# Kernel optimization log

Hardware: AMD Instinct MI355X
Metric: run time of the kernel (lower is better)

The kernel has to match this reference:

```python
import jax, jax.numpy as jnp
import numpy as np

B, T, F, H, NQ = 256, 512, 128, 256, 4


def setup_inputs() -> dict:
    key = jax.random.key(0)
    ks = jax.random.split(key, 7)
    s = 0.1
    return {
        "x": jax.random.normal(ks[0], (B, T, F), dtype=jnp.float32),
        "W_in": jax.random.normal(ks[1], (F + H, NQ), dtype=jnp.float32) * s,
        "b_in": jax.random.normal(ks[2], (NQ,), dtype=jnp.float32) * s,
        "Wq": jax.random.normal(ks[3], (4, NQ, NQ), dtype=jnp.float32) * s,
        "bq": jax.random.normal(ks[4], (4, NQ), dtype=jnp.float32) * s,
        "W_out": jax.random.normal(ks[5], (NQ, H), dtype=jnp.float32) * s,
        "b_out": jax.random.normal(ks[6], (H,), dtype=jnp.float32) * s,
    }


def reference(x, W_in, b_in, Wq, bq, W_out, b_out):
    # x: [B, T, F] (batch_first). Sequential LSTM-like recurrence via lax.scan.
    batch = x.shape[0]
    hidden = W_out.shape[1]

    def step(carry, x_t):
        h, c = carry
        v = jnp.concatenate([h, x_t], axis=1)              # [B, H+F]
        y = v @ W_in + b_in                                # [B, NQ]
        # 4 VQC branches (classical surrogate: tanh(linear)), vectorized over k
        q = jnp.tanh(jnp.einsum('bq,kqr->kbr', y, Wq) + bq[:, None, :])  # [4, B, NQ]
        z = jnp.einsum('kbq,qh->kbh', q, W_out) + b_out    # [4, B, H]
        i = jax.nn.sigmoid(z[0])
        f = jax.nn.sigmoid(z[1])
        g = jnp.tanh(z[2])
        o = jax.nn.sigmoid(z[3])
        c = f * c + i * g
        h = o * jnp.tanh(c)
        return (h, c), h

    h0 = jnp.zeros((batch, hidden), dtype=x.dtype)
    c0 = jnp.zeros((batch, hidden), dtype=x.dtype)
    (h_T, c_T), hs = jax.lax.scan(step, (h0, c0), jnp.swapaxes(x, 0, 1))
    hidden_seq = jnp.swapaxes(hs, 0, 1)                    # [B, T, H]
    return hidden_seq, (h_T, c_T)
```

## Files before the change

### kernel.cpp

```cpp
#include <hip/hip_runtime.h>


#define B_ 256
#define T_ 512
#define F_ 128
#define H_ 256

#define SC1 1.442695041f
#define SC2 2.885390082f
#define ISC2 0.3465735903f

typedef float f2 __attribute__((ext_vector_type(2)));

__device__ __forceinline__ float rcp_f(float x)  { return __builtin_amdgcn_rcpf(x); }
__device__ __forceinline__ float exp2_f(float x) { return __builtin_amdgcn_exp2f(x); }

__device__ __forceinline__ f2 mk2(float a, float b) { f2 v; v.x = a; v.y = b; return v; }

__device__ __forceinline__ float rl(float v, int lane) {
    return __int_as_float(__builtin_amdgcn_readlane(__float_as_int(v), lane));
}

__device__ __forceinline__ void tree4(float& p0, float& p1, float& p2, float& p3) {
    asm volatile(
        "s_nop 1\n\t"
        "v_add_f32_dpp %0, %0, %0 quad_perm:[1,0,3,2] row_mask:0xf bank_mask:0xf\n\t"
        "v_add_f32_dpp %1, %1, %1 quad_perm:[1,0,3,2] row_mask:0xf bank_mask:0xf\n\t"
        "v_add_f32_dpp %2, %2, %2 quad_perm:[1,0,3,2] row_mask:0xf bank_mask:0xf\n\t"
        "v_add_f32_dpp %3, %3, %3 quad_perm:[1,0,3,2] row_mask:0xf bank_mask:0xf\n\t"
        "v_add_f32_dpp %0, %0, %0 quad_perm:[2,3,0,1] row_mask:0xf bank_mask:0xf\n\t"
        "v_add_f32_dpp %1, %1, %1 quad_perm:[2,3,0,1] row_mask:0xf bank_mask:0xf\n\t"
        "v_add_f32_dpp %2, %2, %2 quad_perm:[2,3,0,1] row_mask:0xf bank_mask:0xf\n\t"
        "v_add_f32_dpp %3, %3, %3 quad_perm:[2,3,0,1] row_mask:0xf bank_mask:0xf\n\t"
        "v_add_f32_dpp %0, %0, %0 row_half_mirror row_mask:0xf bank_mask:0xf\n\t"
        "v_add_f32_dpp %1, %1, %1 row_half_mirror row_mask:0xf bank_mask:0xf\n\t"
        "v_add_f32_dpp %2, %2, %2 row_half_mirror row_mask:0xf bank_mask:0xf\n\t"
        "v_add_f32_dpp %3, %3, %3 row_half_mirror row_mask:0xf bank_mask:0xf\n\t"
        "v_add_f32_dpp %0, %0, %0 row_mirror row_mask:0xf bank_mask:0xf\n\t"
        "v_add_f32_dpp %1, %1, %1 row_mirror row_mask:0xf bank_mask:0xf\n\t"
        "v_add_f32_dpp %2, %2, %2 row_mirror row_mask:0xf bank_mask:0xf\n\t"
        "v_add_f32_dpp %3, %3, %3 row_mirror row_mask:0xf bank_mask:0xf\n\t"
        "v_add_f32_dpp %0, %0, %0 row_bcast:15 row_mask:0xf bank_mask:0xf\n\t"
        "v_add_f32_dpp %1, %1, %1 row_bcast:15 row_mask:0xf bank_mask:0xf\n\t"
        "v_add_f32_dpp %2, %2, %2 row_bcast:15 row_mask:0xf bank_mask:0xf\n\t"
        "v_add_f32_dpp %3, %3, %3 row_bcast:15 row_mask:0xf bank_mask:0xf\n\t"
        "v_add_f32_dpp %0, %0, %0 row_bcast:31 row_mask:0xf bank_mask:0xf\n\t"
        "v_add_f32_dpp %1, %1, %1 row_bcast:31 row_mask:0xf bank_mask:0xf\n\t"
        "v_add_f32_dpp %2, %2, %2 row_bcast:31 row_mask:0xf bank_mask:0xf\n\t"
        "v_add_f32_dpp %3, %3, %3 row_bcast:31 row_mask:0xf bank_mask:0xf"
        : "+v"(p0), "+v"(p1), "+v"(p2), "+v"(p3));
}

__device__ __forceinline__ void lds_barrier() {
    asm volatile("s_waitcnt lgkmcnt(0)\n\ts_barrier" ::: "memory");
}

__global__ __launch_bounds__(256, 1) void qlstm_kernel(
    const float* __restrict__ x,
    const float* __restrict__ W_in,
    const float* __restrict__ b_in,
    const float* __restrict__ Wq,
    const float* __restrict__ bq,
    const float* __restrict__ W_out,
    const float* __restrict__ b_out,
    float* __restrict__ out)
{
    const int b = blockIdx.x;
    const int g = threadIdx.x;
    const int w = g >> 6;
    const int l = g & 63;

    __shared__ float4 part[2][4];

    const float4* Win4 = (const float4*)W_in;

    float4 t4 = Win4[g];
    float wh[4] = {t4.x, t4.y, t4.z, t4.w};

    const bool has_x = (w < 2);
    float wx[4] = {0.f, 0.f, 0.f, 0.f};
    if (has_x) {
        float4 u4 = Win4[H_ + g];
        wx[0] = u4.x; wx[1] = u4.y; wx[2] = u4.z; wx[3] = u4.w;
    }

    const float sk[4] = {-SC1, -SC1, SC2, -SC1};
    float wo_k[4][4];
    float bo_k[4];
    {
        const float bo = b_out[g];
#pragma unroll
        for (int r = 0; r < 4; ++r) {
            const float wor = W_out[r * H_ + g];
#pragma unroll
            for (int k = 0; k < 4; ++k) wo_k[k][r] = wor * sk[k];
        }
#pragma unroll
        for (int k = 0; k < 4; ++k) bo_k[k] = bo * sk[k];
    }

    float bin[4];
#pragma unroll
    for (int q = 0; q < 4; ++q) bin[q] = b_in[q];

    const int m = l & 15, qk = m >> 2, qr = m & 3;
    float wql[4];
#pragma unroll
    for (int s = 0; s < 4; ++s) wql[s] = Wq[qk * 16 + s * 4 + qr];
    float bql = bq[qk * 4 + qr];
#pragma unroll
    for (int s = 0; s < 4; ++s) bql = fmaf(bin[s], wql[s], bql);
    bql *= SC2;
#pragma unroll
    for (int s = 0; s < 4; ++s) wql[s] *= SC2;

    float h = 0.f;
    float C = 0.f;

    const float* xp = x + (size_t)b * T_ * F_ + g;
    float xq0 = 0.f, xq1 = 0.f, xq2 = 0.f, xq3 = 0.f;
    float xv1 = 0.f;
    if (has_x) {
        const float xv0 = xp[0];
        xv1 = xp[F_];
        xq0 = xv0 * wx[0]; xq1 = xv0 * wx[1];
        xq2 = xv0 * wx[2]; xq3 = xv0 * wx[3];
    }

    float* outp = out + (size_t)b * T_ * H_ + g;

#define STEP(t, slot)                                                          \
    {                                                                          \
        float p0 = fmaf(h, wh[0], xq0);                                        \
        float p1 = fmaf(h, wh[1], xq1);                                        \
        float p2 = fmaf(h, wh[2], xq2);                                        \
        float p3 = fmaf(h, wh[3], xq3);                                        \
        tree4(p0, p1, p2, p3);                                                 \
        if (l == 63) part[slot][w] = make_float4(p0, p1, p2, p3);              \
        lds_barrier();                                                         \
        const float4 a0 = part[slot][0];                                       \
        const float4 a1 = part[slot][1];                                       \
        const float4 a2 = part[slot][2];                                       \
        const float4 a3 = part[slot][3];                                       \
         \
        if (has_x) {                                                           \
            xq0 = xv1 * wx[0]; xq1 = xv1 * wx[1];                              \
            xq2 = xv1 * wx[2]; xq3 = xv1 * wx[3];                              \
            int tn = (t) + 2; if (tn >= T_) tn = T_ - 1;                       \
            xv1 = xp[(size_t)tn * F_];                                         \
        }                                                                      \
        const f2 y01 = (mk2(a0.x, a0.y) + mk2(a1.x, a1.y)) +                   \
                       (mk2(a2.x, a2.y) + mk2(a3.x, a3.y));                    \
        const f2 y23 = (mk2(a0.z, a0.w) + mk2(a1.z, a1.w)) +                   \
                       (mk2(a2.z, a2.w) + mk2(a3.z, a3.w));                    \
        float u = fmaf(y01.x, wql[0], bql);                                    \
        const float vv = fmaf(y23.x, wql[2], y01.y * wql[1]);                  \
        u = fmaf(y23.y, wql[3], u);                                            \
        const float aq = u + vv;                                               \
        const float qown = 1.0f - 2.0f * rcp_f(1.0f + exp2_f(aq));             \
        float qs[16];                                                          \
        _Pragma("unroll")                                                      \
        for (int i = 0; i < 16; ++i) qs[i] = rl(qown, i);                      \
        float zp[4];                                                           \
        _Pragma("unroll")                                                      \
        for (int k = 0; k < 4; ++k) {                                          \
            float a = fmaf(qs[k * 4 + 0], wo_k[k][0], bo_k[k]);                \
            const float bs = fmaf(qs[k * 4 + 1], wo_k[k][1],                   \
                                  qs[k * 4 + 2] * wo_k[k][2]);                 \
            a = fmaf(qs[k * 4 + 3], wo_k[k][3], a);                            \
            zp[k] = a + bs;                                                    \
        }                                                                      \
        const float e0 = exp2_f(zp[0]);                                        \
        const float e1 = exp2_f(zp[1]);                                        \
        const float E2 = exp2_f(zp[2]);                                        \
        const float e3 = exp2_f(zp[3]);                                        \
        const float num2 = fmaf(SC2, E2, -SC2);                                \
        const float IG2  = num2 * rcp_f((1.0f + e0) * (1.0f + E2));            \
        const float fg   = rcp_f(1.0f + e1);                                   \
        C = fmaf(fg, C, IG2);                                                  \
        const float Ec = exp2_f(C);                                            \
        h = (Ec - 1.0f) * rcp_f((1.0f + e3) * (1.0f + Ec));                    \
        outp[(size_t)(t) * H_] = h;                                            \
    }

    for (int t = 0; t < T_; t += 2) {
        STEP(t, 0);
        STEP(t + 1, 1);
    }
#undef STEP

    float* hT = out + (size_t)B_ * T_ * H_;
    hT[(size_t)b * H_ + g] = h;
    hT[(size_t)B_ * H_ + (size_t)b * H_ + g] = C * ISC2;
}

extern "C" void kernel_launch(void* const* d_in, const int* in_sizes, int n_in,
                              void* d_out, int out_size, void* d_ws, size_t ws_size,
                              hipStream_t stream) {
    const float* x     = (const float*)d_in[0];
    const float* W_in  = (const float*)d_in[1];
    const float* b_in  = (const float*)d_in[2];
    const float* Wq    = (const float*)d_in[3];
    const float* bq    = (const float*)d_in[4];
    const float* W_out = (const float*)d_in[5];
    const float* b_out = (const float*)d_in[6];
    float* out = (float*)d_out;

    qlstm_kernel<<<dim3(B_), dim3(256), 0, stream>>>(
        x, W_in, b_in, Wq, bq, W_out, b_out, out);
}
```

Baseline: 369.9 us.

## Fold Wq projection before LDS exchange and shorten critical-path algebra

Result: no change. 369.9 us (+0.0%).

```diff
diff --git a/kernel.cpp b/kernel.cpp
--- a/kernel.cpp
+++ b/kernel.cpp
@@ -10,12 +10,8 @@
 #define SC2 2.885390082f
 #define ISC2 0.3465735903f
 
-typedef float f2 __attribute__((ext_vector_type(2)));
-
 __device__ __forceinline__ float rcp_f(float x)  { return __builtin_amdgcn_rcpf(x); }
 __device__ __forceinline__ float exp2_f(float x) { return __builtin_amdgcn_exp2f(x); }
-
-__device__ __forceinline__ f2 mk2(float a, float b) { f2 v; v.x = a; v.y = b; return v; }
 
 __device__ __forceinline__ float rl(float v, int lane) {
     return __int_as_float(__builtin_amdgcn_readlane(__float_as_int(v), lane));
@@ -70,7 +66,7 @@
     const int w = g >> 6;
     const int l = g & 63;
 
-    __shared__ float4 part[2][4];
+    __shared__ float partA[2][16][4];
 
     const float4* Win4 = (const float4*)W_in;
 
@@ -85,18 +81,20 @@
     }
 
     const float sk[4] = {-SC1, -SC1, SC2, -SC1};
-    float wo_k[4][4];
-    float bo_k[4];
+    float wo2[4][4];
+    float bo2[4];
     {
         const float bo = b_out[g];
-#pragma unroll
-        for (int r = 0; r < 4; ++r) {
-            const float wor = W_out[r * H_ + g];
-#pragma unroll
-            for (int k = 0; k < 4; ++k) wo_k[k][r] = wor * sk[k];
+        float wos[4];
+        float wsum = 0.f;
+#pragma unroll
+        for (int r = 0; r < 4; ++r) { wos[r] = W_out[r * H_ + g]; wsum += wos[r]; }
+#pragma unroll
+        for (int k = 0; k < 4; ++k) {
+            bo2[k] = sk[k] * (bo + wsum);
+#pragma unroll
+            for (int r = 0; r < 4; ++r) wo2[k][r] = -2.0f * sk[k] * wos[r];
         }
-#pragma unroll
-        for (int k = 0; k < 4; ++k) bo_k[k] = bo * sk[k];
     }
 
     float bin[4];
@@ -113,9 +111,10 @@
     bql *= SC2;
 #pragma unroll
     for (int s = 0; s < 4; ++s) wql[s] *= SC2;
-
-    float h = 0.f;
-    float C = 0.f;
+    const float bqlw = (w == 0) ? bql : 0.0f;
+
+    float tau = 0.f, C = 0.f;
+    float owh0 = 0.f, owh1 = 0.f, owh2 = 0.f, owh3 = 0.f;
 
     const float* xp = x + (size_t)b * T_ * F_ + g;
     float xq0 = 0.f, xq1 = 0.f, xq2 = 0.f, xq3 = 0.f;
@@ -128,20 +127,23 @@
     }
 
     float* outp = out + (size_t)b * T_ * H_ + g;
+    float o_last = 0.f;
 
 #define STEP(t, slot)                                                          \
     {                                                                          \
-        float p0 = fmaf(h, wh[0], xq0);                                        \
-        float p1 = fmaf(h, wh[1], xq1);                                        \
-        float p2 = fmaf(h, wh[2], xq2);                                        \
-        float p3 = fmaf(h, wh[3], xq3);                                        \
+        float p0 = fmaf(tau, owh0, xq0);                                       \
+        float p1 = fmaf(tau, owh1, xq1);                                       \
+        float p2 = fmaf(tau, owh2, xq2);                                       \
+        float p3 = fmaf(tau, owh3, xq3);                                       \
         tree4(p0, p1, p2, p3);                                                 \
-        if (l == 63) part[slot][w] = make_float4(p0, p1, p2, p3);              \
+                \
+        float u = fmaf(p0, wql[0], bqlw);                                      \
+        const float vv = fmaf(p3, wql[3], p2 * wql[2]);                        \
+        u = fmaf(p1, wql[1], u);                                               \
+        const float aqw = u + vv;                                              \
+        if (l >= 48) partA[slot][m][w] = aqw;                                  \
         lds_barrier();                                                         \
-        const float4 a0 = part[slot][0];                                       \
-        const float4 a1 = part[slot][1];                                       \
-        const float4 a2 = part[slot][2];                                       \
-        const float4 a3 = part[slot][3];                                       \
+        const float4 a = *(const float4*)&partA[slot][m][0];                   \
          \
         if (has_x) {                                                           \
             xq0 = xv1 * wx[0]; xq1 = xv1 * wx[1];                              \
@@ -149,26 +151,19 @@
             int tn = (t) + 2; if (tn >= T_) tn = T_ - 1;                       \
             xv1 = xp[(size_t)tn * F_];                                         \
         }                                                                      \
-        const f2 y01 = (mk2(a0.x, a0.y) + mk2(a1.x, a1.y)) +                   \
-                       (mk2(a2.x, a2.y) + mk2(a3.x, a3.y));                    \
-        const f2 y23 = (mk2(a0.z, a0.w) + mk2(a1.z, a1.w)) +                   \
-                       (mk2(a2.z, a2.w) + mk2(a3.z, a3.w));                    \
-        float u = fmaf(y01.x, wql[0], bql);                                    \
-        const float vv = fmaf(y23.x, wql[2], y01.y * wql[1]);                  \
-        u = fmaf(y23.y, wql[3], u);                                            \
-        const float aq = u + vv;                                               \
-        const float qown = 1.0f - 2.0f * rcp_f(1.0f + exp2_f(aq));             \
+        const float aq = (a.x + a.y) + (a.z + a.w);                            \
+        const float qp = rcp_f(1.0f + exp2_f(aq));     \
         float qs[16];                                                          \
         _Pragma("unroll")                                                      \
-        for (int i = 0; i < 16; ++i) qs[i] = rl(qown, i);                      \
+        for (int i = 0; i < 16; ++i) qs[i] = rl(qp, i);                        \
         float zp[4];                                                           \
         _Pragma("unroll")                                                      \
         for (int k = 0; k < 4; ++k) {                                          \
-            float a = fmaf(qs[k * 4 + 0], wo_k[k][0], bo_k[k]);                \
-            const float bs = fmaf(qs[k * 4 + 1], wo_k[k][1],                   \
-                                  qs[k * 4 + 2] * wo_k[k][2]);                 \
-            a = fmaf(qs[k * 4 + 3], wo_k[k][3], a);                            \
-            zp[k] = a + bs;                                                    \
+            float za = fmaf(qs[k * 4 + 0], wo2[k][0], bo2[k]);                 \
+            const float zb = fmaf(qs[k * 4 + 1], wo2[k][1],                    \
+                                  qs[k * 4 + 2] * wo2[k][2]);                  \
+            za = fmaf(qs[k * 4 + 3], wo2[k][3], za);                           \
+            zp[k] = za + zb;                                                   \
         }                                                                      \
         const float e0 = exp2_f(zp[0]);                                        \
         const float e1 = exp2_f(zp[1]);                                        \
@@ -178,9 +173,14 @@
         const float IG2  = num2 * rcp_f((1.0f + e0) * (1.0f + E2));            \
         const float fg   = rcp_f(1.0f + e1);                                   \
         C = fmaf(fg, C, IG2);                                                  \
+                \
+        const float o = rcp_f(1.0f + e3);                                      \
+        owh0 = o * wh[0]; owh1 = o * wh[1];                                    \
+        owh2 = o * wh[2]; owh3 = o * wh[3];                                    \
         const float Ec = exp2_f(C);                                            \
-        h = (Ec - 1.0f) * rcp_f((1.0f + e3) * (1.0f + Ec));                    \
-        outp[(size_t)(t) * H_] = h;                                            \
+        tau = (Ec - 1.0f) * rcp_f(1.0f + Ec);                                  \
+        o_last = o;                                                            \
+        outp[(size_t)(t) * H_] = tau * o;                 \
     }
 
     for (int t = 0; t < T_; t += 2) {
@@ -190,7 +190,7 @@
 #undef STEP
 
     float* hT = out + (size_t)B_ * T_ * H_;
-    hT[(size_t)b * H_ + g] = h;
+    hT[(size_t)b * H_ + g] = tau * o_last;
     hT[(size_t)B_ * H_ + (size_t)b * H_ + g] = C * ISC2;
 }
 
```
